# Performance work log

Hardware: AMD Instinct MI355X
Metric: run time of the kernel (lower is better)

## Reference

```python
import jax, jax.numpy as jnp
import numpy as np

B = 16384
ATOMS_PER = 64
N = B * ATOMS_PER

# 27 periodic-image offsets: all combinations of {-1,0,1}^3 in the module's order
_g = np.array([-1, 0, 1], dtype=np.float32)
OFFSET = np.stack(np.meshgrid(_g, _g, _g, indexing='ij'), axis=-1).reshape(27, 3)


def setup_inputs() -> dict:
    key = jax.random.key(0)
    k1, k2, k3, k4 = jax.random.split(key, 4)
    cell = jax.random.normal(k1, (B, 3, 3), dtype=jnp.float32)
    x = jax.random.uniform(k2, (N, 3), dtype=jnp.float32)
    x_tilde = jax.random.uniform(k3, (N, 3), dtype=jnp.float32)
    x_traj = jax.random.normal(k4, (N, 3), dtype=jnp.float32) * 0.1
    num_atoms = jnp.full((B,), ATOMS_PER, dtype=jnp.int64)
    return {"cell": cell, "x": x, "x_tilde": x_tilde, "x_traj": x_traj,
            "num_atoms": num_atoms}


def reference(cell, x, x_tilde, x_traj, num_atoms):
    # center=True, euclidian=False, distance='l1'
    b = cell.shape[0]
    n = x.shape[0]
    offset = jnp.asarray(OFFSET, dtype=x.dtype)  # [27,3]
    # per-atom structure index (torch repeat_interleave)
    batch = jnp.repeat(jnp.arange(b), num_atoms, total_repeat_length=n)  # [N]
    cell_b = cell[batch]                                    # [N,3,3] gather
    euc_x_tilde = jnp.einsum('nij,nj->ni', cell_b, x_tilde)  # [N,3]
    x_offset = x[:, None, :] + offset[None, :, :]            # [N,27,3]
    euc_x = jnp.einsum('nij,noj->noi', cell_b, x_offset)     # [N,27,3]
    traj = euc_x_tilde[:, None, :] - euc_x                   # [N,27,3]
    dist = jnp.linalg.norm(traj, axis=2)                     # [N,27]
    min_idx = jnp.argmin(dist, axis=1)                       # [N]
    # euclidian=False branch: fractional-space optimal displacement
    sel = jnp.take_along_axis(x_offset, min_idx[:, None, None], axis=1)[:, 0, :]
    optimal_traj = x_tilde - sel                             # [N,3]
    # center=True: subtract per-structure mean (scatter_mean)
    seg_sum = jax.ops.segment_sum(optimal_traj, batch, num_segments=b)  # [B,3]
    seg_mean = seg_sum / num_atoms[:, None].astype(optimal_traj.dtype)
    optimal_traj = optimal_traj - seg_mean[batch]
    # distance='l1'
    return jnp.mean(jnp.abs(x_traj - optimal_traj))
```

## Files before the change

kernel.cpp:

```cpp
#include <hip/hip_runtime.h>


static constexpr int BSTRUCT = 16384;
static constexpr int NATOMS  = BSTRUCT * 64;
static constexpr int BLOCK   = 256;
static constexpr int APT     = 4;
static constexpr int GRID    = NATOMS / (BLOCK * APT);
static constexpr int SPB     = 16;

__global__ __launch_bounds__(BLOCK, 4) void otl_main(
    const float* __restrict__ cell,
    const float* __restrict__ x,
    const float* __restrict__ xt,
    const float* __restrict__ xtr,
    float* __restrict__ partial)
{
    const int t = threadIdx.x;

    __shared__ float cl[SPB * 9];
    __shared__ float sG[SPB][8];
    __shared__ float sQ[SPB][28];

    if (t < SPB * 9) cl[t] = cell[blockIdx.x * (SPB * 9) + t];
    __syncthreads();

    if (t < SPB * 6) {
        const int s = t / 6, e = t - s * 6;
        const int i = (e < 3) ? e : ((e < 5) ? 0 : 1);
        const int j = (e < 3) ? e : ((e == 3) ? 1 : 2);
        const float* c = &cl[s * 9];
        sG[s][e] = c[i] * c[j] + c[3 + i] * c[3 + j] + c[6 + i] * c[6 + j];
    }
    __syncthreads();

    for (int u = t; u < SPB * 27; u += BLOCK) {
        const int s = u / 27, o = u - s * 27;
        const int a = o / 9, r = o - a * 9, b = r / 3, g = r - b * 3;
        const float f1 = (float)(a - 1), f2 = (float)(b - 1), f3 = (float)(g - 1);
        const float* G = sG[s];
        sQ[s][o] = G[0]*f1*f1 + G[1]*f2*f2 + G[2]*f3*f3
                 + 2.0f*(G[3]*f1*f2 + G[4]*f1*f3 + G[5]*f2*f3);
    }
    __syncthreads();

    const int sl = t >> 4;

    float G0,G1,G2,G3,G4,G5;
    {
        const float4 ga = reinterpret_cast<const float4*>(&sG[sl][0])[0];
        const float4 gb = reinterpret_cast<const float4*>(&sG[sl][0])[1];
        G0=ga.x; G1=ga.y; G2=ga.z; G3=ga.w; G4=gb.x; G5=gb.y;
    }
    float q[28];
    #pragma unroll
    for (int i = 0; i < 7; ++i)
        *reinterpret_cast<float4*>(&q[i*4]) =
            reinterpret_cast<const float4*>(&sQ[sl][0])[i];

    const int f4 = (blockIdx.x * BLOCK + t) * 3;
    const float4 xa = reinterpret_cast<const float4*>(x)[f4 + 0];
    const float4 xb = reinterpret_cast<const float4*>(x)[f4 + 1];
    const float4 xc = reinterpret_cast<const float4*>(x)[f4 + 2];
    const float4 ta = reinterpret_cast<const float4*>(xt)[f4 + 0];
    const float4 tb = reinterpret_cast<const float4*>(xt)[f4 + 1];
    const float4 tc = reinterpret_cast<const float4*>(xt)[f4 + 2];

    float dxv[APT], dyv[APT], dzv[APT];
    {
        const float X[12] = {xa.x,xa.y,xa.z,xa.w,xb.x,xb.y,xb.z,xb.w,xc.x,xc.y,xc.z,xc.w};
        const float T[12] = {ta.x,ta.y,ta.z,ta.w,tb.x,tb.y,tb.z,tb.w,tc.x,tc.y,tc.z,tc.w};
        #pragma unroll
        for (int k = 0; k < APT; ++k) {
            dxv[k] = T[k*3+0] - X[k*3+0];
            dyv[k] = T[k*3+1] - X[k*3+1];
            dzv[k] = T[k*3+2] - X[k*3+2];
        }
    }

    float px[APT], py[APT], pz[APT];
    #pragma unroll
    for (int k = 0; k < APT; ++k) {
        const float dx = dxv[k], dy = dyv[k], dz = dzv[k];
        const float w1 = G0*dx + G3*dy + G4*dz;
        const float w2 = G3*dx + G1*dy + G5*dz;
        const float w3 = G4*dx + G5*dy + G2*dz;
        const float wd = w1*dx + w2*dy + w3*dz;
        const float tw1 = w1 + w1, tw2 = w2 + w2, tw3 = w3 + w3;

        float ka[3];
        #pragma unroll
        for (int a = 0; a < 3; ++a) {
            const float sa = (a == 0) ? wd + tw1 : (a == 1) ? wd : wd - tw1;
            float kb[3];
            #pragma unroll
            for (int b = 0; b < 3; ++b) {
                const float sb = (b == 0) ? sa + tw2 : (b == 1) ? sa : sa - tw2;
                const int qo = a*9 + b*3;
                const float d20 = (sb + tw3) + q[qo + 0];
                const float d21 =  sb        + q[qo + 1];
                const float d22 = (sb - tw3) + q[qo + 2];
                const unsigned base = (unsigned)((a << 4) | (b << 2));
                const unsigned k0 = (__float_as_uint(d20) & ~63u) | (base + 0u);
                const unsigned k1 = (__float_as_uint(d21) & ~63u) | (base + 1u);
                const unsigned k2 = (__float_as_uint(d22) & ~63u) | (base + 2u);
                kb[b] = fminf(fminf(__uint_as_float(k0), __uint_as_float(k1)),
                              __uint_as_float(k2));
            }
            ka[a] = fminf(fminf(kb[0], kb[1]), kb[2]);
        }
        const float best = fminf(fminf(ka[0], ka[1]), ka[2]);
        const unsigned bo = __float_as_uint(best) & 63u;
        px[k] = dx - (float)((int)(bo >> 4)        - 1);
        py[k] = dy - (float)((int)((bo >> 2) & 3u) - 1);
        pz[k] = dz - (float)((int)(bo & 3u)        - 1);
    }

    float sx = px[0]+px[1]+px[2]+px[3];
    float sy = py[0]+py[1]+py[2]+py[3];
    float sz = pz[0]+pz[1]+pz[2]+pz[3];
    #pragma unroll
    for (int m = 8; m > 0; m >>= 1) {
        sx += __shfl_xor(sx, m);
        sy += __shfl_xor(sy, m);
        sz += __shfl_xor(sz, m);
    }
    const float inv = 1.0f / 64.0f;
    const float mx = sx*inv, my = sy*inv, mz = sz*inv;

    const float4 ja = reinterpret_cast<const float4*>(xtr)[f4 + 0];
    const float4 jb = reinterpret_cast<const float4*>(xtr)[f4 + 1];
    const float4 jc = reinterpret_cast<const float4*>(xtr)[f4 + 2];
    const float J[12] = {ja.x,ja.y,ja.z,ja.w,jb.x,jb.y,jb.z,jb.w,jc.x,jc.y,jc.z,jc.w};
    float l = 0.0f;
    #pragma unroll
    for (int k = 0; k < APT; ++k) {
        l += fabsf(J[k*3+0] - (px[k]-mx))
           + fabsf(J[k*3+1] - (py[k]-my))
           + fabsf(J[k*3+2] - (pz[k]-mz));
    }

    #pragma unroll
    for (int m = 32; m > 0; m >>= 1) l += __shfl_xor(l, m);

    __shared__ float ls[BLOCK / 64];
    const int lane = t & 63, wave = t >> 6;
    if (lane == 0) ls[wave] = l;
    __syncthreads();
    if (t == 0)
        partial[blockIdx.x] = ls[0] + ls[1] + ls[2] + ls[3];
}

__global__ __launch_bounds__(64) void otl_reduce(
    const float* __restrict__ partial, float* __restrict__ out)
{
    const int t = threadIdx.x;
    const float4* p4 = reinterpret_cast<const float4*>(partial);
    double acc = 0.0;
    #pragma unroll
    for (int i = 0; i < 4; ++i) {
        const float4 p = p4[t * 4 + i];
        acc += (double)p.x + (double)p.y + (double)p.z + (double)p.w;
    }
    #pragma unroll
    for (int m = 32; m > 0; m >>= 1)
        acc += __shfl_xor(acc, m);
    if (t == 0)
        out[0] = (float)(acc / (3.0 * (double)NATOMS));
}

extern "C" void kernel_launch(void* const* d_in, const int* in_sizes, int n_in,
                              void* d_out, int out_size, void* d_ws, size_t ws_size,
                              hipStream_t stream) {
    const float* cell = (const float*)d_in[0];
    const float* x    = (const float*)d_in[1];
    const float* xt   = (const float*)d_in[2];
    const float* xtr  = (const float*)d_in[3];

    float* partials = (float*)d_ws;
    float* out      = (float*)d_out;

    otl_main<<<GRID, BLOCK, 0, stream>>>(cell, x, xt, xtr, partials);
    otl_reduce<<<1, 64, 0, stream>>>(partials, out);
}
```

Baseline: 13.59 us.

## Compute cell metric per thread, drop shared memory and block barriers

Each thread now loads its structure's cell matrix directly and computes the metric tensor and 27 offset norms in registers, removing the shared-memory staging and three __syncthreads. The x_traj load is hoisted to the start to overlap with the other loads, and per-wave partials are written directly instead of being combined through shared memory, so the final reduce reads four times more partials. It trades redundant per-thread ALU work and redundant cell loads for removing barrier stalls.

```diff
diff --git a/kernel.cpp b/kernel.cpp
--- a/kernel.cpp
+++ b/kernel.cpp
@@ -6,7 +6,7 @@
 static constexpr int BLOCK   = 256;
 static constexpr int APT     = 4;
 static constexpr int GRID    = NATOMS / (BLOCK * APT);
-static constexpr int SPB     = 16;
+static constexpr int NPART   = GRID * (BLOCK / 64);
 
 __global__ __launch_bounds__(BLOCK, 4) void otl_main(
     const float* __restrict__ cell,
@@ -16,54 +16,44 @@
     float* __restrict__ partial)
 {
     const int t = threadIdx.x;
+    const int i = blockIdx.x * BLOCK + t;
+    const int s = i >> 4;
 
-    __shared__ float cl[SPB * 9];
-    __shared__ float sG[SPB][8];
-    __shared__ float sQ[SPB][28];
-
-    if (t < SPB * 9) cl[t] = cell[blockIdx.x * (SPB * 9) + t];
-    __syncthreads();
-
-    if (t < SPB * 6) {
-        const int s = t / 6, e = t - s * 6;
-        const int i = (e < 3) ? e : ((e < 5) ? 0 : 1);
-        const int j = (e < 3) ? e : ((e == 3) ? 1 : 2);
-        const float* c = &cl[s * 9];
-        sG[s][e] = c[i] * c[j] + c[3 + i] * c[3 + j] + c[6 + i] * c[6 + j];
-    }
-    __syncthreads();
-
-    for (int u = t; u < SPB * 27; u += BLOCK) {
-        const int s = u / 27, o = u - s * 27;
-        const int a = o / 9, r = o - a * 9, b = r / 3, g = r - b * 3;
-        const float f1 = (float)(a - 1), f2 = (float)(b - 1), f3 = (float)(g - 1);
-        const float* G = sG[s];
-        sQ[s][o] = G[0]*f1*f1 + G[1]*f2*f2 + G[2]*f3*f3
-                 + 2.0f*(G[3]*f1*f2 + G[4]*f1*f3 + G[5]*f2*f3);
-    }
-    __syncthreads();
-
-    const int sl = t >> 4;
-
-    float G0,G1,G2,G3,G4,G5;
-    {
-        const float4 ga = reinterpret_cast<const float4*>(&sG[sl][0])[0];
-        const float4 gb = reinterpret_cast<const float4*>(&sG[sl][0])[1];
-        G0=ga.x; G1=ga.y; G2=ga.z; G3=ga.w; G4=gb.x; G5=gb.y;
-    }
-    float q[28];
-    #pragma unroll
-    for (int i = 0; i < 7; ++i)
-        *reinterpret_cast<float4*>(&q[i*4]) =
-            reinterpret_cast<const float4*>(&sQ[sl][0])[i];
-
-    const int f4 = (blockIdx.x * BLOCK + t) * 3;
+    const int f4 = i * 3;
     const float4 xa = reinterpret_cast<const float4*>(x)[f4 + 0];
     const float4 xb = reinterpret_cast<const float4*>(x)[f4 + 1];
     const float4 xc = reinterpret_cast<const float4*>(x)[f4 + 2];
     const float4 ta = reinterpret_cast<const float4*>(xt)[f4 + 0];
     const float4 tb = reinterpret_cast<const float4*>(xt)[f4 + 1];
     const float4 tc = reinterpret_cast<const float4*>(xt)[f4 + 2];
+    const float4 ja = reinterpret_cast<const float4*>(xtr)[f4 + 0];
+    const float4 jb = reinterpret_cast<const float4*>(xtr)[f4 + 1];
+    const float4 jc = reinterpret_cast<const float4*>(xtr)[f4 + 2];
+
+    const float* c = cell + s * 9;
+    const float c0 = c[0], c1 = c[1], c2 = c[2];
+    const float c3 = c[3], c4 = c[4], c5 = c[5];
+    const float c6 = c[6], c7 = c[7], c8 = c[8];
+
+    const float G0 = c0*c0 + c3*c3 + c6*c6;
+    const float G1 = c1*c1 + c4*c4 + c7*c7;
+    const float G2 = c2*c2 + c5*c5 + c8*c8;
+    const float G3 = c0*c1 + c3*c4 + c6*c7;
+    const float G4 = c0*c2 + c3*c5 + c6*c8;
+    const float G5 = c1*c2 + c4*c5 + c7*c8;
+    const float H3 = G3 + G3, H4 = G4 + G4, H5 = G5 + G5;
+
+    float q[27];
+    #pragma unroll
+    for (int a = 0; a < 3; ++a)
+        #pragma unroll
+        for (int b = 0; b < 3; ++b)
+            #pragma unroll
+            for (int g = 0; g < 3; ++g) {
+                const float fa = (float)(a - 1), fb = (float)(b - 1), fg = (float)(g - 1);
+                q[a*9 + b*3 + g] = G0*fa*fa + G1*fb*fb + G2*fg*fg
+                                 + H3*fa*fb + H4*fa*fg + H5*fb*fg;
+            }
 
     float dxv[APT], dyv[APT], dzv[APT];
     {
@@ -127,9 +117,6 @@
     const float inv = 1.0f / 64.0f;
     const float mx = sx*inv, my = sy*inv, mz = sz*inv;
 
-    const float4 ja = reinterpret_cast<const float4*>(xtr)[f4 + 0];
-    const float4 jb = reinterpret_cast<const float4*>(xtr)[f4 + 1];
-    const float4 jc = reinterpret_cast<const float4*>(xtr)[f4 + 2];
     const float J[12] = {ja.x,ja.y,ja.z,ja.w,jb.x,jb.y,jb.z,jb.w,jc.x,jc.y,jc.z,jc.w};
     float l = 0.0f;
     #pragma unroll
@@ -141,13 +128,8 @@
 
     #pragma unroll
     for (int m = 32; m > 0; m >>= 1) l += __shfl_xor(l, m);
-
-    __shared__ float ls[BLOCK / 64];
-    const int lane = t & 63, wave = t >> 6;
-    if (lane == 0) ls[wave] = l;
-    __syncthreads();
-    if (t == 0)
-        partial[blockIdx.x] = ls[0] + ls[1] + ls[2] + ls[3];
+    if ((t & 63) == 0)
+        partial[(blockIdx.x << 2) | (t >> 6)] = l;
 }
 
 __global__ __launch_bounds__(64) void otl_reduce(
@@ -157,8 +139,8 @@
     const float4* p4 = reinterpret_cast<const float4*>(partial);
     double acc = 0.0;
     #pragma unroll
-    for (int i = 0; i < 4; ++i) {
-        const float4 p = p4[t * 4 + i];
+    for (int i = 0; i < 16; ++i) {
+        const float4 p = p4[t * 16 + i];
         acc += (double)p.x + (double)p.y + (double)p.z + (double)p.w;
     }
     #pragma unroll
```

After: 14.07 us. 3.6% more time.
